# Performance work log

Hardware: AMD Instinct MI355X
Metric: run time of the kernel (lower is better)

The kernel has to match this reference:

```python
import jax, jax.numpy as jnp
import numpy as np

AVG_NOBJ = 49.0
NEG_SLOPE = 0.01  # torch leaky_relu default


def eops_1_to_2(x, nobj, aggregation):
    """x: [B,N,C] -> [B,C,5,N,N] equivariant basis (rank-1 -> rank-2)."""
    B, N, C = x.shape
    xt = jnp.transpose(x, (0, 2, 1))  # B,C,N
    if aggregation == 'sum':
        agg = xt.sum(-1) / AVG_NOBJ                      # B,C
    elif aggregation == 'mean':
        agg = xt.sum(-1) / nobj[:, None]                 # B,C
    elif aggregation == 'max':
        agg = xt.max(-1)
    elif aggregation == 'min':
        agg = xt.min(-1)
    eye = jnp.eye(N, dtype=x.dtype)                      # N,N
    op1 = xt[:, :, :, None] * eye                        # x_i on diagonal
    op2 = jnp.broadcast_to(xt[:, :, None, :], (B, C, N, N))  # x_j along rows
    op3 = jnp.broadcast_to(xt[:, :, :, None], (B, C, N, N))  # x_i along cols
    op4 = agg[:, :, None, None] * eye                    # agg on diagonal
    op5 = jnp.broadcast_to(agg[:, :, None, None], (B, C, N, N))  # agg everywhere
    return jnp.stack([op1, op2, op3, op4, op5], axis=2)  # B,C,5,N,N


def setup_inputs() -> dict:
    key = jax.random.key(0)
    k1, k2 = jax.random.split(key)
    B, N, C, S = 8, 128, 64, 64
    basis_total = 5 * 4  # 5 basis ops per config char, config='smxn'
    inputs = jax.random.normal(k1, (B, N, C), dtype=jnp.float32)
    mask = jnp.ones((B, N, N, 1), dtype=jnp.float32)
    nobj = jnp.full((B,), 100.0, dtype=jnp.float32)
    coefs = jax.random.normal(k2, (C, S, basis_total), dtype=jnp.float32) * np.sqrt(2.0 / (C * basis_total)).astype(np.float32)
    bias = jnp.zeros((S,), dtype=jnp.float32)
    return {"inputs": inputs, "mask": mask, "nobj": nobj, "coefs": coefs, "bias": bias}


def reference(inputs, mask, nobj, coefs, bias):
    # config = 'smxn' -> sum, mean, max, min basis tensors, concat on basis axis
    ops = jnp.concatenate(
        [eops_1_to_2(inputs, nobj, a) for a in ('sum', 'mean', 'max', 'min')],
        axis=2)  # B,C,20,N,N
    out = jnp.einsum('dsb,ndbij->nijs', coefs, ops)      # B,N,N,S
    out = out + bias[None, None, None, :]
    out = jnp.where(out >= 0, out, NEG_SLOPE * out)      # leaky_relu
    return out * mask
```

## Files before the change

### kernel.cpp

```cpp
#include <hip/hip_runtime.h>

constexpr int N = 128, S = 64;
constexpr float INV_AVG = 1.0f / 49.0f;
constexpr float SLOPE = 0.01f;

constexpr int WS_BASE = 0;
constexpr int WS_DIAG = 65536;
constexpr int WS_R    = 131072;

__global__ __launch_bounds__(256) void prep_kernel(
    const float* __restrict__ x,
    const float* __restrict__ nobj,
    const float* __restrict__ coefs,
    const float* __restrict__ bias,
    float* __restrict__ ws)
{
  __shared__ float xs[8192];
  __shared__ float ag[256];
  __shared__ float part[3584];

  const int tid = threadIdx.x;
  const int n   = blockIdx.x >> 5;
  const int i0  = (blockIdx.x & 31) << 2;

  {
    const float4* xg = (const float4*)(x + n * N * 64);
    float4* xs4 = (float4*)xs;
#pragma unroll
    for (int k = 0; k < 8; ++k) xs4[tid + k * 256] = xg[tid + k * 256];
  }
  __syncthreads();

  {
    const int d = tid & 63, grp = tid >> 6;
    float sm = 0.f, mx = -INFINITY, mn = INFINITY;
    for (int i = grp * 32; i < grp * 32 + 32; ++i) {
      float v = xs[i * 64 + d];
      sm += v; mx = fmaxf(mx, v); mn = fminf(mn, v);
    }
    part[grp * 64 + d]       = sm;
    part[256 + grp * 64 + d] = mx;
    part[512 + grp * 64 + d] = mn;
  }
  __syncthreads();
  if (tid < 64) {
    float s0 = part[tid] + part[64 + tid] + part[128 + tid] + part[192 + tid];
    float m0 = fmaxf(fmaxf(part[256 + tid], part[320 + tid]),
                     fmaxf(part[384 + tid], part[448 + tid]));
    float n0 = fminf(fminf(part[512 + tid], part[576 + tid]),
                     fminf(part[640 + tid], part[704 + tid]));
    ag[tid]       = s0 * INV_AVG;
    ag[64 + tid]  = s0 / nobj[n];
    ag[128 + tid] = m0;
    ag[192 + tid] = n0;
  }
  __syncthreads();

  {
    const int g = tid >> 6;
    const int s = tid & 63;
    float pA[4] = {0,0,0,0}, pR[4] = {0,0,0,0}, pC[4] = {0,0,0,0};
    float pD = 0.f, pE = 0.f;
#pragma unroll
    for (int k = 0; k < 16; ++k) {
      const int e = k * 256 + tid;
      const int d = e >> 6;
      const float4* cp = (const float4*)(coefs + e * 20);
      float4 f0 = cp[0], f1 = cp[1], f2 = cp[2], f3 = cp[3], f4v = cp[4];
      float w1v = f0.x + f1.y + f2.z + f3.w;
      float w2v = f0.y + f1.z + f2.w + f4v.x;
      float w3v = f0.z + f1.w + f3.x + f4v.y;
#pragma unroll
      for (int m = 0; m < 4; ++m) {
        float xv = xs[(i0 + m) * 64 + d];
        pA[m] += xv * w1v;
        pR[m] += xv * w2v;
        pC[m] += xv * w3v;
      }
      pD += ag[d] * f0.w + ag[64 + d] * f2.x + ag[128 + d] * f3.y + ag[192 + d] * f4v.z;
      pE += ag[d] * f1.x + ag[64 + d] * f2.y + ag[128 + d] * f3.z + ag[192 + d] * f4v.w;
    }
#pragma unroll
    for (int m = 0; m < 4; ++m) {
      part[m * 256 + g * 64 + s]        = pA[m];
      part[(4 + m) * 256 + g * 64 + s]  = pC[m];
      part[(8 + m) * 256 + g * 64 + s]  = pR[m];
    }
    part[3072 + g * 64 + s] = pD;
    part[3328 + g * 64 + s] = pE;
  }
  __syncthreads();

  if (tid < 64) {
    const int s = tid;
    float D = part[3072 + s] + part[3072 + 64 + s]
            + part[3072 + 128 + s] + part[3072 + 192 + s];
    float E = part[3328 + s] + part[3328 + 64 + s]
            + part[3328 + 128 + s] + part[3328 + 192 + s];
    float bv = bias[s];
#pragma unroll
    for (int m = 0; m < 4; ++m) {
      float A = part[m * 256 + s] + part[m * 256 + 64 + s]
              + part[m * 256 + 128 + s] + part[m * 256 + 192 + s];
      float C = part[(4 + m) * 256 + s] + part[(4 + m) * 256 + 64 + s]
              + part[(4 + m) * 256 + 128 + s] + part[(4 + m) * 256 + 192 + s];
      float R = part[(8 + m) * 256 + s] + part[(8 + m) * 256 + 64 + s]
              + part[(8 + m) * 256 + 128 + s] + part[(8 + m) * 256 + 192 + s];
      const int o = (n * N + i0 + m) * 64 + s;
      ws[WS_BASE + o] = C + E + bv;
      ws[WS_DIAG + o] = A + D;
      ws[WS_R    + o] = R;
    }
  }
}

__global__ __launch_bounds__(256) void assemble_kernel(
    const float* __restrict__ ws,
    const float* __restrict__ mask,
    float* __restrict__ out)
{
  const int g  = blockIdx.x * 256 + threadIdx.x;
  const int l  = g & 15;
  const int p  = g >> 4;
  const int j  = p & 127;
  const int bi = p >> 7;
  const int i  = bi & 127;
  const int n  = bi >> 7;

  const float4* B4 = (const float4*)(ws + WS_BASE);
  const float4* G4 = (const float4*)(ws + WS_DIAG);
  const float4* R4 = (const float4*)(ws + WS_R);

  float4 b = B4[bi * 16 + l];
  float4 r = R4[(n * N + j) * 16 + l];
  float mk = mask[p];

  float v0 = b.x + r.x;
  float v1 = b.y + r.y;
  float v2 = b.z + r.z;
  float v3 = b.w + r.w;
  if (i == j) {
    float4 dg = G4[bi * 16 + l];
    v0 += dg.x; v1 += dg.y; v2 += dg.z; v3 += dg.w;
  }
  v0 = (v0 >= 0.f) ? v0 : SLOPE * v0;
  v1 = (v1 >= 0.f) ? v1 : SLOPE * v1;
  v2 = (v2 >= 0.f) ? v2 : SLOPE * v2;
  v3 = (v3 >= 0.f) ? v3 : SLOPE * v3;

  float4 o;
  o.x = v0 * mk; o.y = v1 * mk; o.z = v2 * mk; o.w = v3 * mk;
  ((float4*)out)[g] = o;
}

extern "C" void kernel_launch(void* const* d_in, const int* in_sizes, int n_in,
                              void* d_out, int out_size, void* d_ws, size_t ws_size,
                              hipStream_t stream) {
  const float* x     = (const float*)d_in[0];
  const float* mask  = (const float*)d_in[1];
  const float* nobj  = (const float*)d_in[2];
  const float* coefs = (const float*)d_in[3];
  const float* bias  = (const float*)d_in[4];
  float* out = (float*)d_out;
  float* ws  = (float*)d_ws;

  prep_kernel<<<256, 256, 0, stream>>>(x, nobj, coefs, bias, ws);
  assemble_kernel<<<8192, 256, 0, stream>>>(ws, mask, out);
}
```

Measured before the change: 81.39 us.

## Fuse prep and assemble into one cooperative kernel with grid sync

Merges the two launches into one cooperative kernel of 1024 blocks. The first 256 blocks compute the per-row workspace, then a grid-wide sync runs, and every block grid-strides over the output in 8 iterations. The x staging in shared memory is removed, so x is read straight from global (cache) memory. This saves one kernel launch and the gap between the kernels, but adds grid-sync cost, and 768 blocks sit idle during the prep phase.

```diff
diff --git a/kernel.cpp b/kernel.cpp
--- a/kernel.cpp
+++ b/kernel.cpp
@@ -1,4 +1,7 @@
 #include <hip/hip_runtime.h>
+#include <hip/hip_cooperative_groups.h>
+
+namespace cg = cooperative_groups;
 
 constexpr int N = 128, S = 64;
 constexpr float INV_AVG = 1.0f / 49.0f;
@@ -8,149 +11,146 @@
 constexpr int WS_DIAG = 65536;
 constexpr int WS_R    = 131072;
 
-__global__ __launch_bounds__(256) void prep_kernel(
+__global__ __launch_bounds__(256, 4) void fused_coop(
     const float* __restrict__ x,
+    const float* __restrict__ mask,
     const float* __restrict__ nobj,
     const float* __restrict__ coefs,
     const float* __restrict__ bias,
-    float* __restrict__ ws)
+    float* __restrict__ ws,
+    float* __restrict__ out)
 {
-  __shared__ float xs[8192];
   __shared__ float ag[256];
   __shared__ float part[3584];
 
   const int tid = threadIdx.x;
-  const int n   = blockIdx.x >> 5;
-  const int i0  = (blockIdx.x & 31) << 2;
 
-  {
-    const float4* xg = (const float4*)(x + n * N * 64);
-    float4* xs4 = (float4*)xs;
+  if (blockIdx.x < 256) {
+    const int n  = blockIdx.x >> 5;
+    const int i0 = (blockIdx.x & 31) << 2;
+
+    {
+      const int d = tid & 63, grp = tid >> 6;
+      float sm = 0.f, mx = -INFINITY, mn = INFINITY;
+#pragma unroll 8
+      for (int i = grp * 32; i < grp * 32 + 32; ++i) {
+        float v = x[(n * N + i) * 64 + d];
+        sm += v; mx = fmaxf(mx, v); mn = fminf(mn, v);
+      }
+      part[grp * 64 + d]       = sm;
+      part[256 + grp * 64 + d] = mx;
+      part[512 + grp * 64 + d] = mn;
+    }
+    __syncthreads();
+    if (tid < 64) {
+      float s0 = part[tid] + part[64 + tid] + part[128 + tid] + part[192 + tid];
+      float m0 = fmaxf(fmaxf(part[256 + tid], part[320 + tid]),
+                       fmaxf(part[384 + tid], part[448 + tid]));
+      float n0 = fminf(fminf(part[512 + tid], part[576 + tid]),
+                       fminf(part[640 + tid], part[704 + tid]));
+      ag[tid]       = s0 * INV_AVG;
+      ag[64 + tid]  = s0 / nobj[n];
+      ag[128 + tid] = m0;
+      ag[192 + tid] = n0;
+    }
+    __syncthreads();
+
+    {
+      const int g = tid >> 6;
+      const int s = tid & 63;
+      float pA[4] = {0,0,0,0}, pR[4] = {0,0,0,0}, pC[4] = {0,0,0,0};
+      float pD = 0.f, pE = 0.f;
 #pragma unroll
-    for (int k = 0; k < 8; ++k) xs4[tid + k * 256] = xg[tid + k * 256];
-  }
-  __syncthreads();
-
-  {
-    const int d = tid & 63, grp = tid >> 6;
-    float sm = 0.f, mx = -INFINITY, mn = INFINITY;
-    for (int i = grp * 32; i < grp * 32 + 32; ++i) {
-      float v = xs[i * 64 + d];
-      sm += v; mx = fmaxf(mx, v); mn = fminf(mn, v);
-    }
-    part[grp * 64 + d]       = sm;
-    part[256 + grp * 64 + d] = mx;
-    part[512 + grp * 64 + d] = mn;
-  }
-  __syncthreads();
-  if (tid < 64) {
-    float s0 = part[tid] + part[64 + tid] + part[128 + tid] + part[192 + tid];
-    float m0 = fmaxf(fmaxf(part[256 + tid], part[320 + tid]),
-                     fmaxf(part[384 + tid], part[448 + tid]));
-    float n0 = fminf(fminf(part[512 + tid], part[576 + tid]),
-                     fminf(part[640 + tid], part[704 + tid]));
-    ag[tid]       = s0 * INV_AVG;
-    ag[64 + tid]  = s0 / nobj[n];
-    ag[128 + tid] = m0;
-    ag[192 + tid] = n0;
-  }
-  __syncthreads();
-
-  {
-    const int g = tid >> 6;
-    const int s = tid & 63;
-    float pA[4] = {0,0,0,0}, pR[4] = {0,0,0,0}, pC[4] = {0,0,0,0};
-    float pD = 0.f, pE = 0.f;
+      for (int k = 0; k < 16; ++k) {
+        const int e = k * 256 + tid;
+        const int d = e >> 6;
+        const float4* cp = (const float4*)(coefs + e * 20);
+        float4 f0 = cp[0], f1 = cp[1], f2 = cp[2], f3 = cp[3], f4v = cp[4];
+        float w1v = f0.x + f1.y + f2.z + f3.w;
+        float w2v = f0.y + f1.z + f2.w + f4v.x;
+        float w3v = f0.z + f1.w + f3.x + f4v.y;
 #pragma unroll
-    for (int k = 0; k < 16; ++k) {
-      const int e = k * 256 + tid;
-      const int d = e >> 6;
-      const float4* cp = (const float4*)(coefs + e * 20);
-      float4 f0 = cp[0], f1 = cp[1], f2 = cp[2], f3 = cp[3], f4v = cp[4];
-      float w1v = f0.x + f1.y + f2.z + f3.w;
-      float w2v = f0.y + f1.z + f2.w + f4v.x;
-      float w3v = f0.z + f1.w + f3.x + f4v.y;
+        for (int m = 0; m < 4; ++m) {
+          float xv = x[(n * N + i0 + m) * 64 + d];
+          pA[m] += xv * w1v;
+          pR[m] += xv * w2v;
+          pC[m] += xv * w3v;
+        }
+        pD += ag[d] * f0.w + ag[64 + d] * f2.x + ag[128 + d] * f3.y + ag[192 + d] * f4v.z;
+        pE += ag[d] * f1.x + ag[64 + d] * f2.y + ag[128 + d] * f3.z + ag[192 + d] * f4v.w;
+      }
 #pragma unroll
       for (int m = 0; m < 4; ++m) {
-        float xv = xs[(i0 + m) * 64 + d];
-        pA[m] += xv * w1v;
-        pR[m] += xv * w2v;
-        pC[m] += xv * w3v;
+        part[m * 256 + g * 64 + s]        = pA[m];
+        part[(4 + m) * 256 + g * 64 + s]  = pC[m];
+        part[(8 + m) * 256 + g * 64 + s]  = pR[m];
       }
-      pD += ag[d] * f0.w + ag[64 + d] * f2.x + ag[128 + d] * f3.y + ag[192 + d] * f4v.z;
-      pE += ag[d] * f1.x + ag[64 + d] * f2.y + ag[128 + d] * f3.z + ag[192 + d] * f4v.w;
+      part[3072 + g * 64 + s] = pD;
+      part[3328 + g * 64 + s] = pE;
     }
+    __syncthreads();
+
+    if (tid < 64) {
+      const int s = tid;
+      float D = part[3072 + s] + part[3072 + 64 + s]
+              + part[3072 + 128 + s] + part[3072 + 192 + s];
+      float E = part[3328 + s] + part[3328 + 64 + s]
+              + part[3328 + 128 + s] + part[3328 + 192 + s];
+      float bv = bias[s];
 #pragma unroll
-    for (int m = 0; m < 4; ++m) {
-      part[m * 256 + g * 64 + s]        = pA[m];
-      part[(4 + m) * 256 + g * 64 + s]  = pC[m];
-      part[(8 + m) * 256 + g * 64 + s]  = pR[m];
-    }
-    part[3072 + g * 64 + s] = pD;
-    part[3328 + g * 64 + s] = pE;
-  }
-  __syncthreads();
-
-  if (tid < 64) {
-    const int s = tid;
-    float D = part[3072 + s] + part[3072 + 64 + s]
-            + part[3072 + 128 + s] + part[3072 + 192 + s];
-    float E = part[3328 + s] + part[3328 + 64 + s]
-            + part[3328 + 128 + s] + part[3328 + 192 + s];
-    float bv = bias[s];
-#pragma unroll
-    for (int m = 0; m < 4; ++m) {
-      float A = part[m * 256 + s] + part[m * 256 + 64 + s]
-              + part[m * 256 + 128 + s] + part[m * 256 + 192 + s];
-      float C = part[(4 + m) * 256 + s] + part[(4 + m) * 256 + 64 + s]
-              + part[(4 + m) * 256 + 128 + s] + part[(4 + m) * 256 + 192 + s];
-      float R = part[(8 + m) * 256 + s] + part[(8 + m) * 256 + 64 + s]
-              + part[(8 + m) * 256 + 128 + s] + part[(8 + m) * 256 + 192 + s];
-      const int o = (n * N + i0 + m) * 64 + s;
-      ws[WS_BASE + o] = C + E + bv;
-      ws[WS_DIAG + o] = A + D;
-      ws[WS_R    + o] = R;
+      for (int m = 0; m < 4; ++m) {
+        float A = part[m * 256 + s] + part[m * 256 + 64 + s]
+                + part[m * 256 + 128 + s] + part[m * 256 + 192 + s];
+        float C = part[(4 + m) * 256 + s] + part[(4 + m) * 256 + 64 + s]
+                + part[(4 + m) * 256 + 128 + s] + part[(4 + m) * 256 + 192 + s];
+        float R = part[(8 + m) * 256 + s] + part[(8 + m) * 256 + 64 + s]
+                + part[(8 + m) * 256 + 128 + s] + part[(8 + m) * 256 + 192 + s];
+        const int o = (n * N + i0 + m) * 64 + s;
+        ws[WS_BASE + o] = C + E + bv;
+        ws[WS_DIAG + o] = A + D;
+        ws[WS_R    + o] = R;
+      }
     }
   }
-}
 
-__global__ __launch_bounds__(256) void assemble_kernel(
-    const float* __restrict__ ws,
-    const float* __restrict__ mask,
-    float* __restrict__ out)
-{
-  const int g  = blockIdx.x * 256 + threadIdx.x;
-  const int l  = g & 15;
-  const int p  = g >> 4;
-  const int j  = p & 127;
-  const int bi = p >> 7;
-  const int i  = bi & 127;
-  const int n  = bi >> 7;
+  cg::this_grid().sync();
 
   const float4* B4 = (const float4*)(ws + WS_BASE);
   const float4* G4 = (const float4*)(ws + WS_DIAG);
   const float4* R4 = (const float4*)(ws + WS_R);
+  const int t0 = blockIdx.x * 256 + tid;
 
-  float4 b = B4[bi * 16 + l];
-  float4 r = R4[(n * N + j) * 16 + l];
-  float mk = mask[p];
+#pragma unroll
+  for (int it = 0; it < 8; ++it) {
+    const int g  = t0 + it * 262144;
+    const int l  = g & 15;
+    const int p  = g >> 4;
+    const int j  = p & 127;
+    const int bi = p >> 7;
+    const int i  = bi & 127;
+    const int n  = bi >> 7;
 
-  float v0 = b.x + r.x;
-  float v1 = b.y + r.y;
-  float v2 = b.z + r.z;
-  float v3 = b.w + r.w;
-  if (i == j) {
-    float4 dg = G4[bi * 16 + l];
-    v0 += dg.x; v1 += dg.y; v2 += dg.z; v3 += dg.w;
+    float4 b = B4[bi * 16 + l];
+    float4 r = R4[(n * N + j) * 16 + l];
+    float mk = mask[p];
+
+    float v0 = b.x + r.x;
+    float v1 = b.y + r.y;
+    float v2 = b.z + r.z;
+    float v3 = b.w + r.w;
+    if (i == j) {
+      float4 dg = G4[bi * 16 + l];
+      v0 += dg.x; v1 += dg.y; v2 += dg.z; v3 += dg.w;
+    }
+    v0 = (v0 >= 0.f) ? v0 : SLOPE * v0;
+    v1 = (v1 >= 0.f) ? v1 : SLOPE * v1;
+    v2 = (v2 >= 0.f) ? v2 : SLOPE * v2;
+    v3 = (v3 >= 0.f) ? v3 : SLOPE * v3;
+
+    float4 o;
+    o.x = v0 * mk; o.y = v1 * mk; o.z = v2 * mk; o.w = v3 * mk;
+    ((float4*)out)[g] = o;
   }
-  v0 = (v0 >= 0.f) ? v0 : SLOPE * v0;
-  v1 = (v1 >= 0.f) ? v1 : SLOPE * v1;
-  v2 = (v2 >= 0.f) ? v2 : SLOPE * v2;
-  v3 = (v3 >= 0.f) ? v3 : SLOPE * v3;
-
-  float4 o;
-  o.x = v0 * mk; o.y = v1 * mk; o.z = v2 * mk; o.w = v3 * mk;
-  ((float4*)out)[g] = o;
 }
 
 extern "C" void kernel_launch(void* const* d_in, const int* in_sizes, int n_in,
@@ -164,6 +164,8 @@
   float* out = (float*)d_out;
   float* ws  = (float*)d_ws;
 
-  prep_kernel<<<256, 256, 0, stream>>>(x, nobj, coefs, bias, ws);
-  assemble_kernel<<<8192, 256, 0, stream>>>(ws, mask, out);
+  void* args[] = { (void*)&x, (void*)&mask, (void*)&nobj, (void*)&coefs,
+                   (void*)&bias, (void*)&ws, (void*)&out };
+  hipLaunchCooperativeKernel((const void*)fused_coop, dim3(1024), dim3(256),
+                             args, 0, stream);
 }
```

After: 211.0 us. 2.59x slower.
